# Kernel tuning notes

Measured on AMD Instinct MI355X. Metric: run time of the kernel, lower is better.

The kernel has to match this reference:

```python
import jax, jax.numpy as jnp
import numpy as np

N_NODES = 50000
N_EDGES = 800000
NFEAT, NHID, NOUT = 128, 128, 64


def _glorot(key, shape):
    lim = 1.0 / np.sqrt(shape[0])
    return jax.random.uniform(key, shape, jnp.float32, -lim, lim)


def setup_inputs() -> dict:
    key = jax.random.key(0)
    ks = jax.random.split(key, 12)
    x = jax.random.normal(ks[0], (N_NODES, NFEAT), jnp.float32)
    edge_src = jax.random.randint(ks[1], (N_EDGES,), 0, N_NODES, jnp.int32)
    edge_dst = jax.random.randint(ks[2], (N_EDGES,), 0, N_NODES, jnp.int32)
    edge_w = jax.random.uniform(ks[3], (N_EDGES,), jnp.float32)  # normalized adj values
    # layer params: nfeat->nhid, nhid->nhid, nhid->nhid, nhid->nout
    W0, b0 = _glorot(ks[4], (NFEAT, NHID)), jnp.zeros((NHID,), jnp.float32)
    W1, b1 = _glorot(ks[5], (NHID, NHID)), jnp.zeros((NHID,), jnp.float32)
    W2, b2 = _glorot(ks[6], (NHID, NHID)), jnp.zeros((NHID,), jnp.float32)
    W3, b3 = _glorot(ks[7], (NHID, NOUT)), jnp.zeros((NOUT,), jnp.float32)
    return dict(x=x, edge_src=edge_src, edge_dst=edge_dst, edge_w=edge_w,
                W0=W0, b0=b0, W1=W1, b1=b1, W2=W2, b2=b2, W3=W3, b3=b3)


def _gcn_layer(h, src, dst, w, W, b):
    # support = h @ W ; out = A @ support + b  (A given as weighted edge list)
    support = h @ W                               # [N, d_out]
    msgs = support[src] * w[:, None]              # [E, d_out] gather + scale
    agg = jax.ops.segment_sum(msgs, dst, num_segments=N_NODES)  # scatter-add
    return agg + b


def reference(x, edge_src, edge_dst, edge_w, W0, b0, W1, b1, W2, b2, W3, b3):
    # eval mode: dropout is identity
    h = jax.nn.relu(_gcn_layer(x, edge_src, edge_dst, edge_w, W0, b0))
    h = jax.nn.relu(_gcn_layer(h, edge_src, edge_dst, edge_w, W1, b1))
    h = jax.nn.relu(_gcn_layer(h, edge_src, edge_dst, edge_w, W2, b2))
    h = _gcn_layer(h, edge_src, edge_dst, edge_w, W3, b3)  # no relu on last layer
    return h
```

## Files before the change

kernel.cpp:

```cpp
#include <hip/hip_runtime.h>


constexpr int NN = 50000;
constexpr int NE = 800000;
constexpr int NB = (NN + 127) >> 7;
constexpr int CAP = 2560;
constexpr int PART_CHUNK = 4096;
constexpr int PART_GRID = (NE + PART_CHUNK - 1) / PART_CHUNK;

typedef __attribute__((ext_vector_type(8))) short bf16x8;
typedef __attribute__((ext_vector_type(4))) float floatx4;

__device__ inline unsigned short f2bf(float f) {
    unsigned u = __float_as_uint(f);
    u += 0x7fffu + ((u >> 16) & 1u);
    return (unsigned short)(u >> 16);
}
__device__ inline float bflo(unsigned v) { return __uint_as_float(v << 16); }
__device__ inline float bfhi(unsigned v) { return __uint_as_float(v & 0xffff0000u); }


__global__ __launch_bounds__(256) void k_part(
        const int* __restrict__ src, const int* __restrict__ dst,
        const float* __restrict__ w, int* __restrict__ bfill,
        int2* __restrict__ ep) {
    __shared__ int hist[NB], base[NB], off[NB];
    int tid = threadIdx.x;
    for (int b = tid; b < NB; b += 256) { hist[b] = 0; off[b] = 0; }
    __syncthreads();

    int e0 = blockIdx.x * PART_CHUNK;
    int  sreg[16]; int wreg[16]; short breg[16];
#pragma unroll
    for (int i = 0; i < 16; ++i) {
        int e = e0 + i * 256 + tid;
        if (e < NE) {
            int d = dst[e];
            int b = d >> 7;
            sreg[i] = (src[e] & 0xffff) | ((d & 127) << 16);
            wreg[i] = __float_as_int(w[e]);
            breg[i] = (short)b;
            atomicAdd(&hist[b], 1);
        } else breg[i] = -1;
    }
    __syncthreads();
    for (int b = tid; b < NB; b += 256)
        base[b] = b * CAP + atomicAdd(&bfill[b], hist[b]);
    __syncthreads();
#pragma unroll
    for (int i = 0; i < 16; ++i) {
        if (breg[i] >= 0) {
            int b = breg[i];
            int p = atomicAdd(&off[b], 1);
            ep[base[b] + p] = make_int2(sreg[i], wreg[i]);
        }
    }
}

__global__ __launch_bounds__(256) void k_sort(
        const int2* __restrict__ ep, const int* __restrict__ bfill,
        int2* __restrict__ es, int2* __restrict__ begend) {
    __shared__ int cnt[128], base[128], fl[128];
    int b  = blockIdx.x;
    int n0 = b << 7;
    int nn = min(128, NN - n0);
    int t  = threadIdx.x;
    if (t < 128) { cnt[t] = 0; fl[t] = 0; }
    __syncthreads();
    int beg = b * CAP, end = beg + bfill[b];
    for (int e = beg + t; e < end; e += 256)
        atomicAdd(&cnt[(ep[e].x >> 16) & 127], 1);
    __syncthreads();
    if (t < 128) base[t] = cnt[t];
    __syncthreads();
    for (int off = 1; off < 128; off <<= 1) {
        int add = (t >= off && t < 128) ? base[t - off] : 0;
        __syncthreads();
        if (t < 128) base[t] += add;
        __syncthreads();
    }
    if (t < nn) begend[n0 + t] = make_int2(beg + base[t] - cnt[t], beg + base[t]);
    __syncthreads();
    for (int e = beg + t; e < end; e += 256) {
        int2 v = ep[e];
        int d = (v.x >> 16) & 127;
        int pos = beg + base[d] - cnt[d] + atomicAdd(&fl[d], 1);
        es[pos] = make_int2(v.x & 0xffff, v.y);
    }
}


__global__ void k_cvtW_all(
        const float* __restrict__ W0, const float* __restrict__ W1,
        const float* __restrict__ W2, const float* __restrict__ W3,
        unsigned short* __restrict__ T0, unsigned short* __restrict__ T1,
        unsigned short* __restrict__ T2, unsigned short* __restrict__ T3) {
    int b = blockIdx.x;
    const float* W; unsigned short* T; int N, n;
    if (b < 128)      { W = W0; T = T0; N = 128; n = b; }
    else if (b < 256) { W = W1; T = T1; N = 128; n = b - 128; }
    else if (b < 384) { W = W2; T = T2; N = 128; n = b - 256; }
    else              { W = W3; T = T3; N = 64;  n = b - 384; }
    int k = threadIdx.x;
    T[n * 128 + k] = f2bf(W[(size_t)k * N + n]);
}


__device__ inline bf16x8 ldA_f32(const float* A, size_t off) {
    float4 u = *(const float4*)&A[off];
    float4 v = *(const float4*)&A[off + 4];
    bf16x8 r;
    r[0] = (short)f2bf(u.x); r[1] = (short)f2bf(u.y);
    r[2] = (short)f2bf(u.z); r[3] = (short)f2bf(u.w);
    r[4] = (short)f2bf(v.x); r[5] = (short)f2bf(v.y);
    r[6] = (short)f2bf(v.z); r[7] = (short)f2bf(v.w);
    return r;
}

__global__ __launch_bounds__(256) void k_gemm0(
        const float* __restrict__ A,
        const unsigned short* __restrict__ Wt,
        unsigned short* __restrict__ C,
        int M) {
    constexpr int STR = 136;
    __shared__ unsigned short sWt[128 * STR];

    const int tid = threadIdx.x;
#pragma unroll
    for (int i = 0; i < 8; ++i) {
        int c = i * 256 + tid;
        int row = c >> 4, col = (c & 15) * 8;
        *(uint4*)&sWt[row * STR + col] = *(const uint4*)&Wt[row * 128 + col];
    }

    const int wv = tid >> 6;
    const int ln = tid & 63;
    const int m  = ln & 15;
    const int qd = ln >> 4;

    int gr  = blockIdx.x * 64 + wv * 16 + m;
    int grc = (gr < M) ? gr : (M - 1);
    bf16x8 af[4];
#pragma unroll
    for (int s = 0; s < 4; ++s)
        af[s] = ldA_f32(A, (size_t)grc * 128 + s * 32 + qd * 8);

    __syncthreads();

    floatx4 acc[8];
#pragma unroll
    for (int c = 0; c < 8; ++c) {
        acc[c] = (floatx4){0.f, 0.f, 0.f, 0.f};
#pragma unroll
        for (int s = 0; s < 4; ++s) {
            bf16x8 bf = *(const bf16x8*)&sWt[(c * 16 + m) * STR + s * 32 + qd * 8];
            acc[c] = __builtin_amdgcn_mfma_f32_16x16x32_bf16(af[s], bf, acc[c], 0, 0, 0);
        }
    }

    int row0 = blockIdx.x * 64 + wv * 16 + qd * 4;
#pragma unroll
    for (int c = 0; c < 8; ++c)
#pragma unroll
        for (int r = 0; r < 4; ++r) {
            int row = row0 + r;
            if (row < M) C[(size_t)row * 128 + c * 16 + m] = f2bf(acc[c][r]);
        }
}


template<int NOUT>
__global__ __launch_bounds__(128, 8) void k_fused(
        const unsigned short* __restrict__ sup,
        const int2* __restrict__ begend, const int2* __restrict__ es,
        const float* __restrict__ bias,
        const unsigned short* __restrict__ Wt,
        unsigned short* __restrict__ C,
        int M) {
    constexpr int NT  = NOUT / 16;
    constexpr int STR = 136;
    __shared__ unsigned short hT[16 * STR];

    const int tid = threadIdx.x;
    const int wv  = tid >> 6;
    const int ln  = tid & 63;
    const int g   = ln >> 4;
    const int l   = ln & 15;

    float bs[8];
#pragma unroll
    for (int f = 0; f < 8; ++f) bs[f] = bias[l * 8 + f];

    const int n0 = blockIdx.x * 16;
    int2 be = begend[n0 + wv * 8];

    for (int nn = 0; nn < 8; ++nn) {
        int n = n0 + wv * 8 + nn;
        int beg = be.x, end = be.y;
        if (nn < 7) be = begend[n + 1];
        float acc[8] = {0.f, 0.f, 0.f, 0.f, 0.f, 0.f, 0.f, 0.f};
        if (end > beg) {
            int e = beg;
            int2 mA = es[min(e + g,     end - 1)];
            int2 mB = es[min(e + 4 + g, end - 1)];
            for (; e + 8 <= end; e += 8) {
                int2 c0 = mA, c1 = mB;
                mA = es[min(e + 8 + g,  end - 1)];
                mB = es[min(e + 12 + g, end - 1)];
                uint4 v0 = *(const uint4*)&sup[(size_t)c0.x * 128 + l * 8];
                uint4 v1 = *(const uint4*)&sup[(size_t)c1.x * 128 + l * 8];
                float w0 = __int_as_float(c0.y), w1 = __int_as_float(c1.y);
                acc[0] = fmaf(w0, bflo(v0.x), acc[0]); acc[1] = fmaf(w0, bfhi(v0.x), acc[1]);
                acc[2] = fmaf(w0, bflo(v0.y), acc[2]); acc[3] = fmaf(w0, bfhi(v0.y), acc[3]);
                acc[4] = fmaf(w0, bflo(v0.z), acc[4]); acc[5] = fmaf(w0, bfhi(v0.z), acc[5]);
                acc[6] = fmaf(w0, bflo(v0.w), acc[6]); acc[7] = fmaf(w0, bfhi(v0.w), acc[7]);
                acc[0] = fmaf(w1, bflo(v1.x), acc[0]); acc[1] = fmaf(w1, bfhi(v1.x), acc[1]);
                acc[2] = fmaf(w1, bflo(v1.y), acc[2]); acc[3] = fmaf(w1, bfhi(v1.y), acc[3]);
                acc[4] = fmaf(w1, bflo(v1.z), acc[4]); acc[5] = fmaf(w1, bfhi(v1.z), acc[5]);
                acc[6] = fmaf(w1, bflo(v1.w), acc[6]); acc[7] = fmaf(w1, bfhi(v1.w), acc[7]);
            }
            if (e < end) {
                uint4 v = *(const uint4*)&sup[(size_t)mA.x * 128 + l * 8];
                float w = (e + g < end) ? __int_as_float(mA.y) : 0.f;
                acc[0] = fmaf(w, bflo(v.x), acc[0]); acc[1] = fmaf(w, bfhi(v.x), acc[1]);
                acc[2] = fmaf(w, bflo(v.y), acc[2]); acc[3] = fmaf(w, bfhi(v.y), acc[3]);
                acc[4] = fmaf(w, bflo(v.z), acc[4]); acc[5] = fmaf(w, bfhi(v.z), acc[5]);
                acc[6] = fmaf(w, bflo(v.w), acc[6]); acc[7] = fmaf(w, bfhi(v.w), acc[7]);
            }
            if (e + 4 < end) {
                uint4 v = *(const uint4*)&sup[(size_t)mB.x * 128 + l * 8];
                float w = (e + 4 + g < end) ? __int_as_float(mB.y) : 0.f;
                acc[0] = fmaf(w, bflo(v.x), acc[0]); acc[1] = fmaf(w, bfhi(v.x), acc[1]);
                acc[2] = fmaf(w, bflo(v.y), acc[2]); acc[3] = fmaf(w, bfhi(v.y), acc[3]);
                acc[4] = fmaf(w, bflo(v.z), acc[4]); acc[5] = fmaf(w, bfhi(v.z), acc[5]);
                acc[6] = fmaf(w, bflo(v.w), acc[6]); acc[7] = fmaf(w, bfhi(v.w), acc[7]);
            }
#pragma unroll
            for (int f = 0; f < 8; ++f) {
                acc[f] += __shfl_xor(acc[f], 16, 64);
                acc[f] += __shfl_xor(acc[f], 32, 64);
            }
        }
        if (g == 0) {
            unsigned pk[4];
#pragma unroll
            for (int q = 0; q < 4; ++q) {
                float a0 = fmaxf(acc[2 * q]     + bs[2 * q],     0.f);
                float a1 = fmaxf(acc[2 * q + 1] + bs[2 * q + 1], 0.f);
                pk[q] = (unsigned)f2bf(a0) | ((unsigned)f2bf(a1) << 16);
            }
            *(uint4*)&hT[(wv * 8 + nn) * STR + l * 8] = *(uint4*)pk;
        }
    }
    __syncthreads();

    const int m_ = ln & 15, qd = ln >> 4;
    const int c0 = wv * (NT / 2);
    bf16x8 af[4];
#pragma unroll
    for (int s = 0; s < 4; ++s)
        af[s] = *(const bf16x8*)&hT[m_ * STR + s * 32 + qd * 8];

    floatx4 acc2[NT / 2];
#pragma unroll
    for (int c = 0; c < NT / 2; ++c) {
        acc2[c] = (floatx4){0.f, 0.f, 0.f, 0.f};
#pragma unroll
        for (int s = 0; s < 4; ++s) {
            bf16x8 bf = *(const bf16x8*)&Wt[(size_t)((c0 + c) * 16 + m_) * 128 + s * 32 + qd * 8];
            acc2[c] = __builtin_amdgcn_mfma_f32_16x16x32_bf16(af[s], bf, acc2[c], 0, 0, 0);
        }
    }
    int row0 = n0 + qd * 4;
#pragma unroll
    for (int c = 0; c < NT / 2; ++c)
#pragma unroll
        for (int r = 0; r < 4; ++r) {
            int row = row0 + r;
            if (row < M) C[(size_t)row * NOUT + (c0 + c) * 16 + m_] = f2bf(acc2[c][r]);
        }
}


__global__ __launch_bounds__(256) void k_agg64(
        const unsigned short* __restrict__ sup,
        const int2* __restrict__ begend, const int2* __restrict__ es,
        const float* __restrict__ bias, float* __restrict__ out) {
    int n  = blockIdx.x * 4 + (threadIdx.x >> 6);
    int ln = threadIdx.x & 63;
    int g  = ln >> 3, l = ln & 7;
    int2 be = begend[n];
    int beg = be.x, end = be.y;
    float acc[8] = {0.f, 0.f, 0.f, 0.f, 0.f, 0.f, 0.f, 0.f};
    if (end > beg) {
        int e = beg;
        int2 mA = es[min(e + g,     end - 1)];
        int2 mB = es[min(e + 8 + g, end - 1)];
        for (; e + 16 <= end; e += 16) {
            int2 c0 = mA, c1 = mB;
            mA = es[min(e + 16 + g, end - 1)];
            mB = es[min(e + 24 + g, end - 1)];
            uint4 v0 = *(const uint4*)&sup[(size_t)c0.x * 64 + l * 8];
            uint4 v1 = *(const uint4*)&sup[(size_t)c1.x * 64 + l * 8];
            float w0 = __int_as_float(c0.y), w1 = __int_as_float(c1.y);
            acc[0] = fmaf(w0, bflo(v0.x), acc[0]); acc[1] = fmaf(w0, bfhi(v0.x), acc[1]);
            acc[2] = fmaf(w0, bflo(v0.y), acc[2]); acc[3] = fmaf(w0, bfhi(v0.y), acc[3]);
            acc[4] = fmaf(w0, bflo(v0.z), acc[4]); acc[5] = fmaf(w0, bfhi(v0.z), acc[5]);
            acc[6] = fmaf(w0, bflo(v0.w), acc[6]); acc[7] = fmaf(w0, bfhi(v0.w), acc[7]);
            acc[0] = fmaf(w1, bflo(v1.x), acc[0]); acc[1] = fmaf(w1, bfhi(v1.x), acc[1]);
            acc[2] = fmaf(w1, bflo(v1.y), acc[2]); acc[3] = fmaf(w1, bfhi(v1.y), acc[3]);
            acc[4] = fmaf(w1, bflo(v1.z), acc[4]); acc[5] = fmaf(w1, bfhi(v1.z), acc[5]);
            acc[6] = fmaf(w1, bflo(v1.w), acc[6]); acc[7] = fmaf(w1, bfhi(v1.w), acc[7]);
        }
        if (e < end) {
            uint4 v = *(const uint4*)&sup[(size_t)mA.x * 64 + l * 8];
            float w = (e + g < end) ? __int_as_float(mA.y) : 0.f;
            acc[0] = fmaf(w, bflo(v.x), acc[0]); acc[1] = fmaf(w, bfhi(v.x), acc[1]);
            acc[2] = fmaf(w, bflo(v.y), acc[2]); acc[3] = fmaf(w, bfhi(v.y), acc[3]);
            acc[4] = fmaf(w, bflo(v.z), acc[4]); acc[5] = fmaf(w, bfhi(v.z), acc[5]);
            acc[6] = fmaf(w, bflo(v.w), acc[6]); acc[7] = fmaf(w, bfhi(v.w), acc[7]);
        }
        if (e + 8 < end) {
            uint4 v = *(const uint4*)&sup[(size_t)mB.x * 64 + l * 8];
            float w = (e + 8 + g < end) ? __int_as_float(mB.y) : 0.f;
            acc[0] = fmaf(w, bflo(v.x), acc[0]); acc[1] = fmaf(w, bfhi(v.x), acc[1]);
            acc[2] = fmaf(w, bflo(v.y), acc[2]); acc[3] = fmaf(w, bfhi(v.y), acc[3]);
            acc[4] = fmaf(w, bflo(v.z), acc[4]); acc[5] = fmaf(w, bfhi(v.z), acc[5]);
            acc[6] = fmaf(w, bflo(v.w), acc[6]); acc[7] = fmaf(w, bfhi(v.w), acc[7]);
        }
    }
#pragma unroll
    for (int f = 0; f < 8; ++f) {
        acc[f] += __shfl_xor(acc[f], 8, 64);
        acc[f] += __shfl_xor(acc[f], 16, 64);
        acc[f] += __shfl_xor(acc[f], 32, 64);
    }
    if (g == 0) {
        float4 o0 = make_float4(acc[0] + bias[l * 8],     acc[1] + bias[l * 8 + 1],
                                acc[2] + bias[l * 8 + 2], acc[3] + bias[l * 8 + 3]);
        float4 o1 = make_float4(acc[4] + bias[l * 8 + 4], acc[5] + bias[l * 8 + 5],
                                acc[6] + bias[l * 8 + 6], acc[7] + bias[l * 8 + 7]);
        *(float4*)&out[(size_t)n * 64 + l * 8]     = o0;
        *(float4*)&out[(size_t)n * 64 + l * 8 + 4] = o1;
    }
}


extern "C" void kernel_launch(void* const* d_in, const int* in_sizes, int n_in,
                              void* d_out, int out_size, void* d_ws, size_t ws_size,
                              hipStream_t stream) {
    (void)in_sizes; (void)n_in; (void)out_size; (void)ws_size;

    const float* x    = (const float*)d_in[0];
    const int*   esrc = (const int*)d_in[1];
    const int*   edst = (const int*)d_in[2];
    const float* ew   = (const float*)d_in[3];
    const float* W0   = (const float*)d_in[4];
    const float* b0   = (const float*)d_in[5];
    const float* W1   = (const float*)d_in[6];
    const float* b1   = (const float*)d_in[7];
    const float* W2   = (const float*)d_in[8];
    const float* b2   = (const float*)d_in[9];
    const float* W3   = (const float*)d_in[10];
    const float* b3   = (const float*)d_in[11];

    char* p = (char*)d_ws;
    auto alloc = [&](size_t bytes) {
        char* r = p;
        p += (bytes + 511) & ~size_t(511);
        return r;
    };
    int*   bfill  = (int*)  alloc((size_t)NB * 4);
    int2*  begend = (int2*) alloc((size_t)NN * 8);
    int2*  ep     = (int2*) alloc((size_t)NB * CAP * 8);
    int2*  es     = (int2*) alloc((size_t)NB * CAP * 8);
    unsigned short* sA  = (unsigned short*)alloc((size_t)NN * 128 * 2);
    unsigned short* sB  = (unsigned short*)alloc((size_t)NN * 128 * 2);
    unsigned short* Wt0 = (unsigned short*)alloc((size_t)128 * 128 * 2);
    unsigned short* Wt1 = (unsigned short*)alloc((size_t)128 * 128 * 2);
    unsigned short* Wt2 = (unsigned short*)alloc((size_t)128 * 128 * 2);
    unsigned short* Wt3 = (unsigned short*)alloc((size_t)64 * 128 * 2);

    hipMemsetAsync(bfill, 0, (size_t)NB * 4, stream);
    k_part<<<PART_GRID, 256, 0, stream>>>(esrc, edst, ew, bfill, ep);
    k_sort<<<NB, 256, 0, stream>>>(ep, bfill, es, begend);

    k_cvtW_all<<<448, 128, 0, stream>>>(W0, W1, W2, W3, Wt0, Wt1, Wt2, Wt3);

    const int g0_grid = (NN + 63) / 64;
    const int f_grid  = (NN + 15) / 16;
    const int a_grid  = (NN + 3) / 4;

    k_gemm0<<<g0_grid, 256, 0, stream>>>(x, Wt0, sA, NN);
    k_fused<128><<<f_grid, 128, 0, stream>>>(sA, begend, es, b0, Wt1, sB, NN);
    k_fused<128><<<f_grid, 128, 0, stream>>>(sB, begend, es, b1, Wt2, sA, NN);
    k_fused<64><<<f_grid, 128, 0, stream>>>(sA, begend, es, b2, Wt3, sB, NN);
    k_agg64<<<a_grid, 256, 0, stream>>>(sB, begend, es, b3, (float*)d_out);
}
```

Baseline: 258.1 us.

## Software-pipeline feature gathers in aggregation loops and fold memset into weight prep

The aggregation loops in the fused and final kernels now issue the gather of the next batch of support rows before doing the FMAs on the current batch. This double buffers the feature loads as well as the edge metadata, so gather latency overlaps with arithmetic. The tail handling is merged into the loop by zeroing the weights of out-of-range edges. Separately, the bucket-counter memset moves into the weight-conversion kernel as an extra block, removing one launch, at the cost of more live registers.

Measured after the change: 263.0 us. About the same (+1.9%).

```diff
diff --git a/kernel.cpp b/kernel.cpp
--- a/kernel.cpp
+++ b/kernel.cpp
@@ -90,12 +90,17 @@
 }
 
 
-__global__ void k_cvtW_all(
+__global__ void k_prep(
         const float* __restrict__ W0, const float* __restrict__ W1,
         const float* __restrict__ W2, const float* __restrict__ W3,
         unsigned short* __restrict__ T0, unsigned short* __restrict__ T1,
-        unsigned short* __restrict__ T2, unsigned short* __restrict__ T3) {
+        unsigned short* __restrict__ T2, unsigned short* __restrict__ T3,
+        int* __restrict__ bfill) {
     int b = blockIdx.x;
+    if (b == 448) {
+        for (int i = threadIdx.x; i < NB; i += 128) bfill[i] = 0;
+        return;
+    }
     const float* W; unsigned short* T; int N, n;
     if (b < 128)      { W = W0; T = T0; N = 128; n = b; }
     else if (b < 256) { W = W1; T = T1; N = 128; n = b - 128; }
@@ -201,39 +206,35 @@
         float acc[8] = {0.f, 0.f, 0.f, 0.f, 0.f, 0.f, 0.f, 0.f};
         if (end > beg) {
             int e = beg;
-            int2 mA = es[min(e + g,     end - 1)];
-            int2 mB = es[min(e + 4 + g, end - 1)];
-            for (; e + 8 <= end; e += 8) {
-                int2 c0 = mA, c1 = mB;
-                mA = es[min(e + 8 + g,  end - 1)];
-                mB = es[min(e + 12 + g, end - 1)];
-                uint4 v0 = *(const uint4*)&sup[(size_t)c0.x * 128 + l * 8];
-                uint4 v1 = *(const uint4*)&sup[(size_t)c1.x * 128 + l * 8];
-                float w0 = __int_as_float(c0.y), w1 = __int_as_float(c1.y);
-                acc[0] = fmaf(w0, bflo(v0.x), acc[0]); acc[1] = fmaf(w0, bfhi(v0.x), acc[1]);
-                acc[2] = fmaf(w0, bflo(v0.y), acc[2]); acc[3] = fmaf(w0, bfhi(v0.y), acc[3]);
-                acc[4] = fmaf(w0, bflo(v0.z), acc[4]); acc[5] = fmaf(w0, bfhi(v0.z), acc[5]);
-                acc[6] = fmaf(w0, bflo(v0.w), acc[6]); acc[7] = fmaf(w0, bfhi(v0.w), acc[7]);
-                acc[0] = fmaf(w1, bflo(v1.x), acc[0]); acc[1] = fmaf(w1, bfhi(v1.x), acc[1]);
-                acc[2] = fmaf(w1, bflo(v1.y), acc[2]); acc[3] = fmaf(w1, bfhi(v1.y), acc[3]);
-                acc[4] = fmaf(w1, bflo(v1.z), acc[4]); acc[5] = fmaf(w1, bfhi(v1.z), acc[5]);
-                acc[6] = fmaf(w1, bflo(v1.w), acc[6]); acc[7] = fmaf(w1, bfhi(v1.w), acc[7]);
-            }
-            if (e < end) {
-                uint4 v = *(const uint4*)&sup[(size_t)mA.x * 128 + l * 8];
-                float w = (e + g < end) ? __int_as_float(mA.y) : 0.f;
-                acc[0] = fmaf(w, bflo(v.x), acc[0]); acc[1] = fmaf(w, bfhi(v.x), acc[1]);
-                acc[2] = fmaf(w, bflo(v.y), acc[2]); acc[3] = fmaf(w, bfhi(v.y), acc[3]);
-                acc[4] = fmaf(w, bflo(v.z), acc[4]); acc[5] = fmaf(w, bfhi(v.z), acc[5]);
-                acc[6] = fmaf(w, bflo(v.w), acc[6]); acc[7] = fmaf(w, bfhi(v.w), acc[7]);
-            }
-            if (e + 4 < end) {
-                uint4 v = *(const uint4*)&sup[(size_t)mB.x * 128 + l * 8];
-                float w = (e + 4 + g < end) ? __int_as_float(mB.y) : 0.f;
-                acc[0] = fmaf(w, bflo(v.x), acc[0]); acc[1] = fmaf(w, bfhi(v.x), acc[1]);
-                acc[2] = fmaf(w, bflo(v.y), acc[2]); acc[3] = fmaf(w, bfhi(v.y), acc[3]);
-                acc[4] = fmaf(w, bflo(v.z), acc[4]); acc[5] = fmaf(w, bfhi(v.z), acc[5]);
-                acc[6] = fmaf(w, bflo(v.w), acc[6]); acc[7] = fmaf(w, bfhi(v.w), acc[7]);
+            int2 mA0 = es[min(e + g,      end - 1)];
+            int2 mB0 = es[min(e + 4 + g,  end - 1)];
+            int2 mA1 = es[min(e + 8 + g,  end - 1)];
+            int2 mB1 = es[min(e + 12 + g, end - 1)];
+            uint4 r0 = *(const uint4*)&sup[(size_t)mA0.x * 128 + l * 8];
+            uint4 r1 = *(const uint4*)&sup[(size_t)mB0.x * 128 + l * 8];
+            for (;;) {
+                float w0 = (e + g     < end) ? __int_as_float(mA0.y) : 0.f;
+                float w1 = (e + 4 + g < end) ? __int_as_float(mB0.y) : 0.f;
+                bool more = (e + 8) < end;
+                uint4 s0, s1;
+                if (more) {
+                    s0 = *(const uint4*)&sup[(size_t)mA1.x * 128 + l * 8];
+                    s1 = *(const uint4*)&sup[(size_t)mB1.x * 128 + l * 8];
+                    mA0 = mA1; mB0 = mB1;
+                    mA1 = es[min(e + 16 + g, end - 1)];
+                    mB1 = es[min(e + 20 + g, end - 1)];
+                }
+                acc[0] = fmaf(w0, bflo(r0.x), acc[0]); acc[1] = fmaf(w0, bfhi(r0.x), acc[1]);
+                acc[2] = fmaf(w0, bflo(r0.y), acc[2]); acc[3] = fmaf(w0, bfhi(r0.y), acc[3]);
+                acc[4] = fmaf(w0, bflo(r0.z), acc[4]); acc[5] = fmaf(w0, bfhi(r0.z), acc[5]);
+                acc[6] = fmaf(w0, bflo(r0.w), acc[6]); acc[7] = fmaf(w0, bfhi(r0.w), acc[7]);
+                acc[0] = fmaf(w1, bflo(r1.x), acc[0]); acc[1] = fmaf(w1, bfhi(r1.x), acc[1]);
+                acc[2] = fmaf(w1, bflo(r1.y), acc[2]); acc[3] = fmaf(w1, bfhi(r1.y), acc[3]);
+                acc[4] = fmaf(w1, bflo(r1.z), acc[4]); acc[5] = fmaf(w1, bfhi(r1.z), acc[5]);
+                acc[6] = fmaf(w1, bflo(r1.w), acc[6]); acc[7] = fmaf(w1, bfhi(r1.w), acc[7]);
+                if (!more) break;
+                r0 = s0; r1 = s1;
+                e += 8;
             }
 #pragma unroll
             for (int f = 0; f < 8; ++f) {
@@ -294,39 +295,35 @@
     float acc[8] = {0.f, 0.f, 0.f, 0.f, 0.f, 0.f, 0.f, 0.f};
     if (end > beg) {
         int e = beg;
-        int2 mA = es[min(e + g,     end - 1)];
-        int2 mB = es[min(e + 8 + g, end - 1)];
-        for (; e + 16 <= end; e += 16) {
-            int2 c0 = mA, c1 = mB;
-            mA = es[min(e + 16 + g, end - 1)];
-            mB = es[min(e + 24 + g, end - 1)];
-            uint4 v0 = *(const uint4*)&sup[(size_t)c0.x * 64 + l * 8];
-            uint4 v1 = *(const uint4*)&sup[(size_t)c1.x * 64 + l * 8];
-            float w0 = __int_as_float(c0.y), w1 = __int_as_float(c1.y);
-            acc[0] = fmaf(w0, bflo(v0.x), acc[0]); acc[1] = fmaf(w0, bfhi(v0.x), acc[1]);
-            acc[2] = fmaf(w0, bflo(v0.y), acc[2]); acc[3] = fmaf(w0, bfhi(v0.y), acc[3]);
-            acc[4] = fmaf(w0, bflo(v0.z), acc[4]); acc[5] = fmaf(w0, bfhi(v0.z), acc[5]);
-            acc[6] = fmaf(w0, bflo(v0.w), acc[6]); acc[7] = fmaf(w0, bfhi(v0.w), acc[7]);
-            acc[0] = fmaf(w1, bflo(v1.x), acc[0]); acc[1] = fmaf(w1, bfhi(v1.x), acc[1]);
-            acc[2] = fmaf(w1, bflo(v1.y), acc[2]); acc[3] = fmaf(w1, bfhi(v1.y), acc[3]);
-            acc[4] = fmaf(w1, bflo(v1.z), acc[4]); acc[5] = fmaf(w1, bfhi(v1.z), acc[5]);
-            acc[6] = fmaf(w1, bflo(v1.w), acc[6]); acc[7] = fmaf(w1, bfhi(v1.w), acc[7]);
-        }
-        if (e < end) {
-            uint4 v = *(const uint4*)&sup[(size_t)mA.x * 64 + l * 8];
-            float w = (e + g < end) ? __int_as_float(mA.y) : 0.f;
-            acc[0] = fmaf(w, bflo(v.x), acc[0]); acc[1] = fmaf(w, bfhi(v.x), acc[1]);
-            acc[2] = fmaf(w, bflo(v.y), acc[2]); acc[3] = fmaf(w, bfhi(v.y), acc[3]);
-            acc[4] = fmaf(w, bflo(v.z), acc[4]); acc[5] = fmaf(w, bfhi(v.z), acc[5]);
-            acc[6] = fmaf(w, bflo(v.w), acc[6]); acc[7] = fmaf(w, bfhi(v.w), acc[7]);
-        }
-        if (e + 8 < end) {
-            uint4 v = *(const uint4*)&sup[(size_t)mB.x * 64 + l * 8];
-            float w = (e + 8 + g < end) ? __int_as_float(mB.y) : 0.f;
-            acc[0] = fmaf(w, bflo(v.x), acc[0]); acc[1] = fmaf(w, bfhi(v.x), acc[1]);
-            acc[2] = fmaf(w, bflo(v.y), acc[2]); acc[3] = fmaf(w, bfhi(v.y), acc[3]);
-            acc[4] = fmaf(w, bflo(v.z), acc[4]); acc[5] = fmaf(w, bfhi(v.z), acc[5]);
-            acc[6] = fmaf(w, bflo(v.w), acc[6]); acc[7] = fmaf(w, bfhi(v.w), acc[7]);
+        int2 mA0 = es[min(e + g,      end - 1)];
+        int2 mB0 = es[min(e + 8 + g,  end - 1)];
+        int2 mA1 = es[min(e + 16 + g, end - 1)];
+        int2 mB1 = es[min(e + 24 + g, end - 1)];
+        uint4 r0 = *(const uint4*)&sup[(size_t)mA0.x * 64 + l * 8];
+        uint4 r1 = *(const uint4*)&sup[(size_t)mB0.x * 64 + l * 8];
+        for (;;) {
+            float w0 = (e + g     < end) ? __int_as_float(mA0.y) : 0.f;
+            float w1 = (e + 8 + g < end) ? __int_as_float(mB0.y) : 0.f;
+            bool more = (e + 16) < end;
+            uint4 s0, s1;
+            if (more) {
+                s0 = *(const uint4*)&sup[(size_t)mA1.x * 64 + l * 8];
+                s1 = *(const uint4*)&sup[(size_t)mB1.x * 64 + l * 8];
+                mA0 = mA1; mB0 = mB1;
+                mA1 = es[min(e + 32 + g, end - 1)];
+                mB1 = es[min(e + 40 + g, end - 1)];
+            }
+            acc[0] = fmaf(w0, bflo(r0.x), acc[0]); acc[1] = fmaf(w0, bfhi(r0.x), acc[1]);
+            acc[2] = fmaf(w0, bflo(r0.y), acc[2]); acc[3] = fmaf(w0, bfhi(r0.y), acc[3]);
+            acc[4] = fmaf(w0, bflo(r0.z), acc[4]); acc[5] = fmaf(w0, bfhi(r0.z), acc[5]);
+            acc[6] = fmaf(w0, bflo(r0.w), acc[6]); acc[7] = fmaf(w0, bfhi(r0.w), acc[7]);
+            acc[0] = fmaf(w1, bflo(r1.x), acc[0]); acc[1] = fmaf(w1, bfhi(r1.x), acc[1]);
+            acc[2] = fmaf(w1, bflo(r1.y), acc[2]); acc[3] = fmaf(w1, bfhi(r1.y), acc[3]);
+            acc[4] = fmaf(w1, bflo(r1.z), acc[4]); acc[5] = fmaf(w1, bfhi(r1.z), acc[5]);
+            acc[6] = fmaf(w1, bflo(r1.w), acc[6]); acc[7] = fmaf(w1, bfhi(r1.w), acc[7]);
+            if (!more) break;
+            r0 = s0; r1 = s1;
+            e += 16;
         }
     }
 #pragma unroll
@@ -381,11 +378,9 @@
     unsigned short* Wt2 = (unsigned short*)alloc((size_t)128 * 128 * 2);
     unsigned short* Wt3 = (unsigned short*)alloc((size_t)64 * 128 * 2);
 
-    hipMemsetAsync(bfill, 0, (size_t)NB * 4, stream);
+    k_prep<<<449, 128, 0, stream>>>(W0, W1, W2, W3, Wt0, Wt1, Wt2, Wt3, bfill);
     k_part<<<PART_GRID, 256, 0, stream>>>(esrc, edst, ew, bfill, ep);
     k_sort<<<NB, 256, 0, stream>>>(ep, bfill, es, begend);
-
-    k_cvtW_all<<<448, 128, 0, stream>>>(W0, W1, W2, W3, Wt0, Wt1, Wt2, Wt3);
 
     const int g0_grid = (NN + 63) / 64;
     const int f_grid  = (NN + 15) / 16;
```
